# Optimization experiments

Measured on AMD Instinct MI355X. Metric: run time of the kernel, lower is better.

The kernel has to match this reference:

```python
import jax, jax.numpy as jnp
import numpy as np

B, N, D = 4, 4096, 1024
H, HD = 16, 64            # num_heads, head_dim (dim // num_heads)
K_ANCHOR = 256
SCALE = 1.0 / np.sqrt(float(HD))


def setup_inputs() -> dict:
    key = jax.random.key(0)
    ks = jax.random.split(key, 12)
    init = lambda k, shape, fan_in: jax.random.normal(k, shape, jnp.float32) * (1.0 / np.sqrt(fan_in))
    return {
        "x": jax.random.normal(ks[0], (B, N, D), jnp.float32),
        "Wq": init(ks[1], (D, H * HD), D), "bq": jnp.zeros((H * HD,), jnp.float32),
        "Wk": init(ks[2], (D, H * HD), D), "bk": jnp.zeros((H * HD,), jnp.float32),
        "Wv": init(ks[3], (D, H * HD), D), "bv": jnp.zeros((H * HD,), jnp.float32),
        "Wqt": init(ks[4], (D, D), D),     "bqt": jnp.zeros((D,), jnp.float32),
        "Wo": init(ks[5], (H * HD, D), H * HD), "bo": jnp.zeros((D,), jnp.float32),
        "num_anchor_tokens": K_ANCHOR,
    }


def _split_heads(t):
    # [B, S, H*HD] -> [B, H, S, HD]
    b, s, _ = t.shape
    return t.reshape(b, s, H, HD).transpose(0, 2, 1, 3)


def reference(x, Wq, bq, Wk, bk, Wv, bv, Wqt, bqt, Wo, bo, num_anchor_tokens):
    K = num_anchor_tokens  # static python int
    anchors = x[:, :K]     # [B, K, D]
    queries = x[:, K:]     # [B, N-K, D]

    q_a = anchors @ Wq + bq           # [B, K, H*HD]
    k_a = anchors @ Wk + bk           # [B, K, H*HD]
    v_a = anchors @ Wv + bv           # [B, K, H*HD]
    q_q = queries @ Wqt + bqt         # [B, N-K, H*HD] (dim == H*HD)

    q = _split_heads(jnp.concatenate([q_a, q_q], axis=1))  # [B, H, N, HD]
    k = _split_heads(k_a)                                  # [B, H, K, HD]
    v = _split_heads(v_a)                                  # [B, H, K, HD]

    scores = jnp.einsum("bhnd,bhkd->bhnk", q, k) * SCALE   # [B, H, N, K]
    weights = jax.nn.softmax(scores, axis=-1)
    ctx = jnp.einsum("bhnk,bhkd->bhnd", weights, v)        # [B, H, N, HD]
    ctx = ctx.transpose(0, 2, 1, 3).reshape(x.shape[0], x.shape[1], H * HD)
    return ctx @ Wo + bo               # [B, N, D]
```

## Files before the change

kernel.cpp:

```cpp
#include <hip/hip_runtime.h>
#include <stdint.h>
#include <stddef.h>


typedef _Float16 v8hf __attribute__((ext_vector_type(8)));
typedef _Float16 h4   __attribute__((ext_vector_type(4)));
typedef float    f32x4 __attribute__((ext_vector_type(4)));
typedef uint32_t u32x4 __attribute__((ext_vector_type(4)));

#define ATT_SCALE 0.125f
#define LOG2E     1.44269504088896340736f
#define QK_CE     (ATT_SCALE * LOG2E)

__device__ __forceinline__ void async16(const void* g, void* l) {
  __builtin_amdgcn_global_load_lds(
      (const __attribute__((address_space(1))) void*)g,
      (__attribute__((address_space(3))) void*)l,
      16, 0, 0);
}

__device__ __forceinline__ uint32_t pk_h2(float a, float b) {
  auto w = __builtin_amdgcn_cvt_pkrtz(a, b);
  return __builtin_bit_cast(uint32_t, w);
}

__global__ __launch_bounds__(256) void cvt_kernel(const float* __restrict__ src,
                                                  _Float16* __restrict__ dst, int n) {
  int i = (blockIdx.x * 256 + threadIdx.x) * 4;
  if (i + 3 < n) {
    float4 v = *(const float4*)(src + i);
    h4 o; o[0] = (_Float16)v.x; o[1] = (_Float16)v.y; o[2] = (_Float16)v.z; o[3] = (_Float16)v.w;
    *(h4*)(dst + i) = o;
  }
}

struct TPArgs { const float* src[5]; _Float16* dst[5]; };

__global__ __launch_bounds__(256) void transpose5_k(TPArgs a) {
  __shared__ _Float16 t[32][33];
  const int z = blockIdx.z;
  const float* __restrict__ src = a.src[z];
  _Float16* __restrict__ dst = a.dst[z];
  const int bx = blockIdx.x * 32, by = blockIdx.y * 32;
  const int x = threadIdx.x;
  for (int yy = threadIdx.y; yy < 32; yy += 8)
    t[yy][x] = (_Float16)src[(size_t)(by + yy) * 1024 + bx + x];
  __syncthreads();
  for (int yy = threadIdx.y; yy < 32; yy += 8)
    dst[(size_t)(bx + yy) * 1024 + by + x] = t[x][yy];
}

template <typename OutT>
__global__ __launch_bounds__(512, 2) void gemm256(
    const _Float16* __restrict__ A, const _Float16* __restrict__ Bt,
    const float* __restrict__ bias, OutT* __restrict__ out,
    int rowsPerBatch, int rowStart, float oscale)
{
  __shared__ __attribute__((aligned(16))) _Float16 As[4 * 256 * 32];
  __shared__ __attribute__((aligned(16))) _Float16 Bs[4 * 256 * 32];

  const int tid  = threadIdx.x;
  const int wave = tid >> 6, lane = tid & 63;
  const int quad = lane >> 4, l16 = lane & 15;
  const int wr = wave >> 2, wc = wave & 3;

  const int nwg = gridDim.x * gridDim.y;
  const int lin = blockIdx.y * 4 + blockIdx.x;
  const int swz = (lin & 7) * (nwg >> 3) + (lin >> 3);
  const int bx = swz & 3, by = swz >> 2;

  const int lrow = lane >> 2, lblk = lane & 3;

  auto gRowOf = [&](int m) -> int {
    int b = m / rowsPerBatch;
    return b * 4096 + rowStart + (m - b * rowsPerBatch);
  };

  const int tr0 = wave * 16 + lrow;
  const int tr1 = 128 + tr0;
  const _Float16* aS0 = A  + (size_t)gRowOf(by * 256 + tr0) * 1024 + (lblk ^ ((tr0 >> 1) & 3)) * 8;
  const _Float16* aS1 = A  + (size_t)gRowOf(by * 256 + tr1) * 1024 + (lblk ^ ((tr1 >> 1) & 3)) * 8;
  const _Float16* bS0 = Bt + (size_t)(bx * 256 + tr0) * 1024 + (lblk ^ ((tr0 >> 1) & 3)) * 8;
  const _Float16* bS1 = Bt + (size_t)(bx * 256 + tr1) * 1024 + (lblk ^ ((tr1 >> 1) & 3)) * 8;

  auto stageA = [&](int t) {
    const int k0 = t * 32;
    _Float16* ad = As + (t & 3) * 8192 + wave * 512;
    async16(aS0 + k0, ad);
    async16(aS1 + k0, ad + 4096);
  };
  auto stageB = [&](int t) {
    const int k0 = t * 32;
    _Float16* bd = Bs + (t & 3) * 8192 + wave * 512;
    async16(bS0 + k0, bd);
    async16(bS1 + k0, bd + 4096);
  };

  const int fblk = (quad ^ ((l16 >> 1) & 3)) * 8;

  f32x4 acc[8][4];
  #pragma unroll
  for (int i = 0; i < 8; i++)
    #pragma unroll
    for (int j = 0; j < 4; j++)
      acc[i][j] = f32x4{0.f, 0.f, 0.f, 0.f};

  stageA(0); stageB(0); stageA(1); stageB(1); stageA(2); stageB(2);
  asm volatile("s_waitcnt vmcnt(8)" ::: "memory");
  __builtin_amdgcn_s_barrier();

  #pragma unroll 1
  for (int t = 0; t < 32; ++t) {
    const _Float16* Ab = As + (t & 3) * 8192;
    const _Float16* Bb = Bs + (t & 3) * 8192;
    v8hf af0[4], af1[4], bf[4];

    #pragma unroll
    for (int nt = 0; nt < 4; nt++)
      bf[nt] = *(const v8hf*)(Bb + (wc * 64 + nt * 16 + l16) * 32 + fblk);
    #pragma unroll
    for (int mt = 0; mt < 4; mt++)
      af0[mt] = *(const v8hf*)(Ab + (wr * 128 + mt * 16 + l16) * 32 + fblk);
    if (t + 3 < 32) stageA(t + 3);
    __builtin_amdgcn_s_barrier();
    asm volatile("s_waitcnt lgkmcnt(0)" ::: "memory");
    __builtin_amdgcn_sched_barrier(0);
    __builtin_amdgcn_s_setprio(1);
    #pragma unroll
    for (int mt = 0; mt < 4; mt++)
      #pragma unroll
      for (int nt = 0; nt < 4; nt++)
        acc[mt][nt] = __builtin_amdgcn_mfma_f32_16x16x32_f16(af0[mt], bf[nt], acc[mt][nt], 0, 0, 0);
    __builtin_amdgcn_s_setprio(0);
    __builtin_amdgcn_s_barrier();

    #pragma unroll
    for (int mt = 0; mt < 4; mt++)
      af1[mt] = *(const v8hf*)(Ab + (wr * 128 + (mt + 4) * 16 + l16) * 32 + fblk);
    if (t + 3 < 32) stageB(t + 3);
    if (t <= 28)      asm volatile("s_waitcnt vmcnt(6)" ::: "memory");
    else if (t == 29) asm volatile("s_waitcnt vmcnt(4)" ::: "memory");
    else              asm volatile("s_waitcnt vmcnt(0)" ::: "memory");
    __builtin_amdgcn_s_barrier();
    asm volatile("s_waitcnt lgkmcnt(0)" ::: "memory");
    __builtin_amdgcn_sched_barrier(0);
    __builtin_amdgcn_s_setprio(1);
    #pragma unroll
    for (int mt = 0; mt < 4; mt++)
      #pragma unroll
      for (int nt = 0; nt < 4; nt++)
        acc[mt + 4][nt] = __builtin_amdgcn_mfma_f32_16x16x32_f16(af1[mt], bf[nt], acc[mt + 4][nt], 0, 0, 0);
    __builtin_amdgcn_s_setprio(0);
    __builtin_amdgcn_s_barrier();
  }

  const int colBase = bx * 256 + wc * 64;
  const int rowBase = by * 256 + wr * 128;
  #pragma unroll
  for (int mt = 0; mt < 8; mt++) {
    #pragma unroll
    for (int r = 0; r < 4; r++) {
      int m = rowBase + mt * 16 + quad * 4 + r;
      int b = m / rowsPerBatch;
      int rr = m - b * rowsPerBatch;
      #pragma unroll
      for (int nt = 0; nt < 4; nt++) {
        int col = colBase + nt * 16 + l16;
        float v = (acc[mt][nt][r] + bias[col]) * oscale;
        out[(size_t)(b * 4096 + rowStart + rr) * 1024 + col] = (OutT)v;
      }
    }
  }
}

template <typename OutT>
__global__ __launch_bounds__(256) void gemm64(
    const _Float16* __restrict__ A, const _Float16* __restrict__ Bt,
    const float* __restrict__ bias0, const float* __restrict__ bias1,
    const float* __restrict__ bias2,
    OutT* __restrict__ out0, _Float16* __restrict__ out1, _Float16* __restrict__ out2,
    int rowsPerBatch, int rowStart, int mode)
{
  __shared__ __attribute__((aligned(16))) _Float16 As[64 * 32];
  __shared__ __attribute__((aligned(16))) _Float16 Bs[128 * 32];

  const int tid  = threadIdx.x;
  const int wave = tid >> 6, lane = tid & 63;
  const int quad = lane >> 4, l16 = lane & 15;
  const int wr = wave >> 1, wc = wave & 1;

  const int gx = gridDim.x;
  const int lin = blockIdx.y * gx + blockIdx.x;
  const int x8 = lin & 7, j = lin >> 3;
  const int bx = j % gx;
  const int by = x8 * (gridDim.y >> 3) + j / gx;

  const int srow = lane >> 2;
  const int skol = (((lane & 3) ^ ((lane >> 3) & 3)) * 8);

  auto gRowOf = [&](int m) -> int {
    int b = m / rowsPerBatch;
    int r = m - b * rowsPerBatch;
    return b * 4096 + rowStart + r;
  };

  const int bc0 = wave * 2, bc1 = bc0 + 1;
  const _Float16* aS  = A  + (size_t)gRowOf(by * 64 + wave * 16 + srow) * 1024 + skol;
  const _Float16* bS0 = Bt + (size_t)(bx * 128 + bc0 * 16 + srow) * 1024 + skol;
  const _Float16* bS1 = Bt + (size_t)(bx * 128 + bc1 * 16 + srow) * 1024 + skol;
  _Float16* aD  = As + wave * 512;
  _Float16* bD0 = Bs + bc0 * 512;
  _Float16* bD1 = Bs + bc1 * 512;

  const int fblk = (quad ^ ((l16 >> 1) & 3)) * 8;

  f32x4 acc[2][4];
  #pragma unroll
  for (int i = 0; i < 2; i++)
    #pragma unroll
    for (int jj = 0; jj < 4; jj++)
      acc[i][jj] = f32x4{0.f, 0.f, 0.f, 0.f};

  for (int k0 = 0; k0 < 1024; k0 += 32) {
    __syncthreads();
    async16(aS  + k0, aD);
    async16(bS0 + k0, bD0);
    async16(bS1 + k0, bD1);
    __syncthreads();

    v8hf af[2], bfr[4];
    #pragma unroll
    for (int mt = 0; mt < 2; mt++)
      af[mt] = *(const v8hf*)(As + (wr * 32 + mt * 16 + l16) * 32 + fblk);
    #pragma unroll
    for (int nt = 0; nt < 4; nt++)
      bfr[nt] = *(const v8hf*)(Bs + (wc * 64 + nt * 16 + l16) * 32 + fblk);
    #pragma unroll
    for (int mt = 0; mt < 2; mt++)
      #pragma unroll
      for (int nt = 0; nt < 4; nt++)
        acc[mt][nt] = __builtin_amdgcn_mfma_f32_16x16x32_f16(af[mt], bfr[nt], acc[mt][nt], 0, 0, 0);
  }

  const int colBase = bx * 128 + wc * 64;
  const int rowBase = by * 64 + wr * 32;
  #pragma unroll
  for (int mt = 0; mt < 2; mt++) {
    #pragma unroll
    for (int r = 0; r < 4; r++) {
      int m = rowBase + mt * 16 + quad * 4 + r;
      int b = m / rowsPerBatch;
      int rr = m - b * rowsPerBatch;
      #pragma unroll
      for (int nt = 0; nt < 4; nt++) {
        int col = colBase + nt * 16 + l16;
        float v = acc[mt][nt][r];
        if (mode == 0) {
          v += bias0[col];
          out0[(size_t)(b * 4096 + rowStart + rr) * 1024 + col] = (OutT)v;
        } else {
          if (col < 1024) {
            v = (v + bias0[col]) * QK_CE;
            out0[(size_t)(b * 4096 + rr) * 1024 + col] = (OutT)v;
          } else if (col < 2048) {
            int c2 = col - 1024;
            v += bias1[c2];
            out1[(size_t)(b * 256 + rr) * 1024 + c2] = (_Float16)v;
          } else {
            int c2 = col - 2048;
            v += bias2[c2];
            int hh = c2 >> 6, d = c2 & 63;
            int kk = ((rr >> 7) & 1) * 128 + (rr & 15) * 8 + ((rr >> 4) & 7);
            int idx = ((kk >> 5) * 4 + (d >> 4)) * 512
                    + (((kk >> 3) & 3) * 16 + (d & 15)) * 8 + (kk & 7);
            out2[(size_t)(b * 16 + hh) * 16384 + idx] = (_Float16)v;
          }
        }
      }
    }
  }
}

__global__ __launch_bounds__(256, 5) void attn_kernel(
    const _Float16* __restrict__ q, const _Float16* __restrict__ k,
    const _Float16* __restrict__ vt, _Float16* __restrict__ ctx)
{
  __shared__ __attribute__((aligned(16))) _Float16 KP[256 * 64];

  const int tid  = threadIdx.x;
  const int wave = tid >> 6, lane = tid & 63;
  const int quad = lane >> 4, l16 = lane & 15;
  const int bid = blockIdx.x;
  const int qt = bid & 63, h = (bid >> 6) & 15, b = bid >> 10;

  const int fq = (l16 ^ (l16 >> 1)) & 7;

  const _Float16* kbase = k + (size_t)b * 256 * 1024 + h * 64;
  {
    const int s = lane >> 3;
    const int p = lane & 7;
    #pragma unroll
    for (int i = 0; i < 8; i++) {
      int c = wave * 8 + i;
      int row = c * 8 + s;
      int f = (row ^ (row >> 1)) & 7;
      async16(kbase + (size_t)row * 1024 + (p ^ f) * 8, KP + c * 512);
    }
  }

  const int qrow = qt * 64 + wave * 16 + l16;
  const _Float16* qbase = q + (size_t)(b * 4096 + qrow) * 1024 + h * 64 + quad * 8;
  v8hf a0 = *(const v8hf*)(qbase);
  v8hf a1 = *(const v8hf*)(qbase + 32);

  f32x4 s[16];
  #pragma unroll
  for (int t = 0; t < 16; t++) s[t] = f32x4{0.f, 0.f, 0.f, 0.f};

  __syncthreads();

  #pragma unroll
  for (int t = 0; t < 16; t++) {
    const _Float16* rbase = KP + (t * 16 + l16) * 64;
    int pb0 = (quad ^ fq) * 8;
    v8hf b0 = *(const v8hf*)(rbase + pb0);
    v8hf b1 = *(const v8hf*)(rbase + (pb0 ^ 32));
    s[t] = __builtin_amdgcn_mfma_f32_16x16x32_f16(a0, b0, s[t], 0, 0, 0);
    s[t] = __builtin_amdgcn_mfma_f32_16x16x32_f16(a1, b1, s[t], 0, 0, 0);
  }

  float inv[4];
  #pragma unroll
  for (int r = 0; r < 4; r++) {
    float sum = 0.f;
    #pragma unroll
    for (int t = 0; t < 16; t++) {
      float e = __builtin_amdgcn_exp2f(s[t][r]);
      s[t][r] = e;
      sum += e;
    }
    sum += __shfl_xor(sum, 1);
    sum += __shfl_xor(sum, 2);
    sum += __shfl_xor(sum, 4);
    sum += __shfl_xor(sum, 8);
    inv[r] = 1.0f / sum;
  }

  __syncthreads();

  #pragma unroll
  for (int r = 0; r < 4; r++) {
    const int qr = quad * 4 + r;
    const int fp = (qr ^ (qr >> 1)) & 7;
    _Float16* prow = KP + (wave * 16 + qr) * 256;
    u32x4 lo, hi;
    #pragma unroll
    for (int j = 0; j < 4; j++) {
      lo[j] = pk_h2(s[2 * j][r],     s[2 * j + 1][r]);
      hi[j] = pk_h2(s[2 * j + 8][r], s[2 * j + 9][r]);
    }
    *(u32x4*)(prow + (l16 ^ fp) * 8)        = lo;
    *(u32x4*)(prow + ((l16 ^ fp) + 16) * 8) = hi;
  }

  asm volatile("s_waitcnt lgkmcnt(0)" ::: "memory");
  __builtin_amdgcn_sched_barrier(0);

  const _Float16* vlane = vt + (size_t)(b * 16 + h) * 16384 + lane * 8;
  f32x4 o[4];
  #pragma unroll
  for (int nt = 0; nt < 4; nt++) o[nt] = f32x4{0.f, 0.f, 0.f, 0.f};
  #pragma unroll
  for (int c = 0; c < 8; c++) {
    v8hf pa = *(const v8hf*)(KP + (wave * 16 + l16) * 256 + ((c * 4 + quad) ^ fq) * 8);
    #pragma unroll
    for (int nt = 0; nt < 4; nt++) {
      v8hf vb = *(const v8hf*)(vlane + (c * 4 + nt) * 512);
      o[nt] = __builtin_amdgcn_mfma_f32_16x16x32_f16(pa, vb, o[nt], 0, 0, 0);
    }
  }

  _Float16* obase = ctx + (size_t)(b * 4096 + qt * 64 + wave * 16 + quad * 4) * 1024 + h * 64;
  #pragma unroll
  for (int nt = 0; nt < 4; nt++)
    #pragma unroll
    for (int r = 0; r < 4; r++)
      obase[(size_t)r * 1024 + nt * 16 + l16] = (_Float16)(o[nt][r] * inv[r]);
}

extern "C" void kernel_launch(void* const* d_in, const int* in_sizes, int n_in,
                              void* d_out, int out_size, void* d_ws, size_t ws_size,
                              hipStream_t stream)
{
  (void)in_sizes; (void)n_in; (void)out_size; (void)ws_size;

  const float* x   = (const float*)d_in[0];
  const float* Wq  = (const float*)d_in[1];
  const float* bq  = (const float*)d_in[2];
  const float* Wk  = (const float*)d_in[3];
  const float* bk  = (const float*)d_in[4];
  const float* Wv  = (const float*)d_in[5];
  const float* bv  = (const float*)d_in[6];
  const float* Wqt = (const float*)d_in[7];
  const float* bqt = (const float*)d_in[8];
  const float* Wo  = (const float*)d_in[9];
  const float* bo  = (const float*)d_in[10];

  char* ws = (char*)d_ws;
  _Float16* xh    = (_Float16*)(ws);
  _Float16* WtQKV = (_Float16*)(ws + (32ll << 20));
  _Float16* WtQT  = (_Float16*)(ws + (38ll << 20));
  _Float16* WtO   = (_Float16*)(ws + (40ll << 20));
  _Float16* qbuf  = (_Float16*)(ws + (42ll << 20));
  _Float16* kbuf  = (_Float16*)(ws + (74ll << 20));
  _Float16* vtb   = (_Float16*)(ws + (76ll << 20));
  _Float16* ctxb  = (_Float16*)(ws + (78ll << 20));
  float* outp = (float*)d_out;

  const int nx = 4 * 4096 * 1024;
  cvt_kernel<<<nx / 1024, 256, 0, stream>>>(x, xh, nx);

  TPArgs tpa;
  tpa.src[0] = Wq;  tpa.dst[0] = WtQKV;
  tpa.src[1] = Wk;  tpa.dst[1] = WtQKV + 1024 * 1024;
  tpa.src[2] = Wv;  tpa.dst[2] = WtQKV + 2 * 1024 * 1024;
  tpa.src[3] = Wqt; tpa.dst[3] = WtQT;
  tpa.src[4] = Wo;  tpa.dst[4] = WtO;
  transpose5_k<<<dim3(32, 32, 5), dim3(32, 8), 0, stream>>>(tpa);

  gemm64<_Float16><<<dim3(24, 16), 256, 0, stream>>>(xh, WtQKV, bq, bk, bv,
                                                     qbuf, kbuf, vtb, 256, 0, 1);
  gemm256<_Float16><<<dim3(4, 60), 512, 0, stream>>>(xh, WtQT, bqt,
                                                     qbuf, 3840, 256, QK_CE);
  attn_kernel<<<4096, 256, 0, stream>>>(qbuf, kbuf, vtb, ctxb);
  gemm256<float><<<dim3(4, 64), 512, 0, stream>>>(ctxb, WtO, bo,
                                                  outp, 4096, 0, 1.0f);
}
```

Baseline: 289.2 us.

## Merge prep kernels and fuse anchor QKV and query projections into one GEMM launch

```diff
diff --git a/kernel.cpp b/kernel.cpp
--- a/kernel.cpp
+++ b/kernel.cpp
@@ -24,30 +24,32 @@
   return __builtin_bit_cast(uint32_t, w);
 }
 
-__global__ __launch_bounds__(256) void cvt_kernel(const float* __restrict__ src,
-                                                  _Float16* __restrict__ dst, int n) {
-  int i = (blockIdx.x * 256 + threadIdx.x) * 4;
-  if (i + 3 < n) {
-    float4 v = *(const float4*)(src + i);
+struct TPArgs { const float* src[5]; _Float16* dst[5]; };
+
+__global__ __launch_bounds__(256) void prep_kernel(
+    const float* __restrict__ x, _Float16* __restrict__ xh, TPArgs a)
+{
+  __shared__ _Float16 t[32][33];
+  const int bid = blockIdx.x;
+  if (bid < 16384) {
+    int i = (bid * 256 + threadIdx.x) * 4;
+    float4 v = *(const float4*)(x + i);
     h4 o; o[0] = (_Float16)v.x; o[1] = (_Float16)v.y; o[2] = (_Float16)v.z; o[3] = (_Float16)v.w;
-    *(h4*)(dst + i) = o;
-  }
-}
-
-struct TPArgs { const float* src[5]; _Float16* dst[5]; };
-
-__global__ __launch_bounds__(256) void transpose5_k(TPArgs a) {
-  __shared__ _Float16 t[32][33];
-  const int z = blockIdx.z;
-  const float* __restrict__ src = a.src[z];
-  _Float16* __restrict__ dst = a.dst[z];
-  const int bx = blockIdx.x * 32, by = blockIdx.y * 32;
-  const int x = threadIdx.x;
-  for (int yy = threadIdx.y; yy < 32; yy += 8)
-    t[yy][x] = (_Float16)src[(size_t)(by + yy) * 1024 + bx + x];
-  __syncthreads();
-  for (int yy = threadIdx.y; yy < 32; yy += 8)
-    dst[(size_t)(bx + yy) * 1024 + by + x] = t[x][yy];
+    *(h4*)(xh + i) = o;
+  } else {
+    const int tb = bid - 16384;
+    const int z = tb >> 10;
+    const int rem = tb & 1023;
+    const int bxx = (rem & 31) * 32, byy = (rem >> 5) * 32;
+    const float* __restrict__ src = a.src[z];
+    _Float16* __restrict__ dst = a.dst[z];
+    const int xx = threadIdx.x & 31, ty = threadIdx.x >> 5;
+    for (int yy = ty; yy < 32; yy += 8)
+      t[yy][xx] = (_Float16)src[(size_t)(byy + yy) * 1024 + bxx + xx];
+    __syncthreads();
+    for (int yy = ty; yy < 32; yy += 8)
+      dst[(size_t)(bxx + yy) * 1024 + byy + xx] = t[xx][yy];
+  }
 }
 
 template <typename OutT>
@@ -173,79 +175,123 @@
   }
 }
 
-template <typename OutT>
-__global__ __launch_bounds__(256) void gemm64(
-    const _Float16* __restrict__ A, const _Float16* __restrict__ Bt,
-    const float* __restrict__ bias0, const float* __restrict__ bias1,
-    const float* __restrict__ bias2,
-    OutT* __restrict__ out0, _Float16* __restrict__ out1, _Float16* __restrict__ out2,
-    int rowsPerBatch, int rowStart, int mode)
+__global__ __launch_bounds__(512, 2) void gemm_qkv(
+    const _Float16* __restrict__ xh,
+    const _Float16* __restrict__ WtQT, const _Float16* __restrict__ WtQKV,
+    const float* __restrict__ bqt, const float* __restrict__ bq,
+    const float* __restrict__ bk, const float* __restrict__ bv,
+    _Float16* __restrict__ qout, _Float16* __restrict__ kout,
+    _Float16* __restrict__ vout)
 {
-  __shared__ __attribute__((aligned(16))) _Float16 As[64 * 32];
-  __shared__ __attribute__((aligned(16))) _Float16 Bs[128 * 32];
+  __shared__ __attribute__((aligned(16))) _Float16 As[4 * 256 * 32];
+  __shared__ __attribute__((aligned(16))) _Float16 Bs[4 * 256 * 32];
 
   const int tid  = threadIdx.x;
   const int wave = tid >> 6, lane = tid & 63;
   const int quad = lane >> 4, l16 = lane & 15;
-  const int wr = wave >> 1, wc = wave & 1;
-
-  const int gx = gridDim.x;
-  const int lin = blockIdx.y * gx + blockIdx.x;
-  const int x8 = lin & 7, j = lin >> 3;
-  const int bx = j % gx;
-  const int by = x8 * (gridDim.y >> 3) + j / gx;
-
-  const int srow = lane >> 2;
-  const int skol = (((lane & 3) ^ ((lane >> 3) & 3)) * 8);
+  const int wr = wave >> 2, wc = wave & 3;
+
+  const int nwg = gridDim.x;
+  const int lin = blockIdx.x;
+  const int swz = (lin & 7) * (nwg >> 3) + (lin >> 3);
+  const bool anch = swz >= 240;
+  const int id = anch ? (swz - 240) : swz;
+  const int bx = anch ? (id % 12) : (id & 3);
+  const int by = anch ? (id / 12) : (id >> 2);
+
+  const _Float16* __restrict__ Bt = anch ? WtQKV : WtQT;
+  const int rowsPerBatch = anch ? 256 : 3840;
+  const int rowStart     = anch ? 0 : 256;
+
+  const int lrow = lane >> 2, lblk = lane & 3;
 
   auto gRowOf = [&](int m) -> int {
     int b = m / rowsPerBatch;
-    int r = m - b * rowsPerBatch;
-    return b * 4096 + rowStart + r;
-  };
-
-  const int bc0 = wave * 2, bc1 = bc0 + 1;
-  const _Float16* aS  = A  + (size_t)gRowOf(by * 64 + wave * 16 + srow) * 1024 + skol;
-  const _Float16* bS0 = Bt + (size_t)(bx * 128 + bc0 * 16 + srow) * 1024 + skol;
-  const _Float16* bS1 = Bt + (size_t)(bx * 128 + bc1 * 16 + srow) * 1024 + skol;
-  _Float16* aD  = As + wave * 512;
-  _Float16* bD0 = Bs + bc0 * 512;
-  _Float16* bD1 = Bs + bc1 * 512;
+    return b * 4096 + rowStart + (m - b * rowsPerBatch);
+  };
+
+  const int tr0 = wave * 16 + lrow;
+  const int tr1 = 128 + tr0;
+  const _Float16* aS0 = xh + (size_t)gRowOf(by * 256 + tr0) * 1024 + (lblk ^ ((tr0 >> 1) & 3)) * 8;
+  const _Float16* aS1 = xh + (size_t)gRowOf(by * 256 + tr1) * 1024 + (lblk ^ ((tr1 >> 1) & 3)) * 8;
+  const _Float16* bS0 = Bt + (size_t)(bx * 256 + tr0) * 1024 + (lblk ^ ((tr0 >> 1) & 3)) * 8;
+  const _Float16* bS1 = Bt + (size_t)(bx * 256 + tr1) * 1024 + (lblk ^ ((tr1 >> 1) & 3)) * 8;
+
+  auto stageA = [&](int t) {
+    const int k0 = t * 32;
+    _Float16* ad = As + (t & 3) * 8192 + wave * 512;
+    async16(aS0 + k0, ad);
+    async16(aS1 + k0, ad + 4096);
+  };
+  auto stageB = [&](int t) {
+    const int k0 = t * 32;
+    _Float16* bd = Bs + (t & 3) * 8192 + wave * 512;
+    async16(bS0 + k0, bd);
+    async16(bS1 + k0, bd + 4096);
+  };
 
   const int fblk = (quad ^ ((l16 >> 1) & 3)) * 8;
 
-  f32x4 acc[2][4];
-  #pragma unroll
-  for (int i = 0; i < 2; i++)
-    #pragma unroll
-    for (int jj = 0; jj < 4; jj++)
-      acc[i][jj] = f32x4{0.f, 0.f, 0.f, 0.f};
-
-  for (int k0 = 0; k0 < 1024; k0 += 32) {
-    __syncthreads();
-    async16(aS  + k0, aD);
-    async16(bS0 + k0, bD0);
-    async16(bS1 + k0, bD1);
-    __syncthreads();
-
-    v8hf af[2], bfr[4];
-    #pragma unroll
-    for (int mt = 0; mt < 2; mt++)
-      af[mt] = *(const v8hf*)(As + (wr * 32 + mt * 16 + l16) * 32 + fblk);
+  f32x4 acc[8][4];
+  #pragma unroll
+  for (int i = 0; i < 8; i++)
+    #pragma unroll
+    for (int j = 0; j < 4; j++)
+      acc[i][j] = f32x4{0.f, 0.f, 0.f, 0.f};
+
+  stageA(0); stageB(0); stageA(1); stageB(1); stageA(2); stageB(2);
+  asm volatile("s_waitcnt vmcnt(8)" ::: "memory");
+  __builtin_amdgcn_s_barrier();
+
+  #pragma unroll 1
+  for (int t = 0; t < 32; ++t) {
+    const _Float16* Ab = As + (t & 3) * 8192;
+    const _Float16* Bb = Bs + (t & 3) * 8192;
+    v8hf af0[4], af1[4], bf[4];
+
     #pragma unroll
     for (int nt = 0; nt < 4; nt++)
-      bfr[nt] = *(const v8hf*)(Bs + (wc * 64 + nt * 16 + l16) * 32 + fblk);
-    #pragma unroll
-    for (int mt = 0; mt < 2; mt++)
+      bf[nt] = *(const v8hf*)(Bb + (wc * 64 + nt * 16 + l16) * 32 + fblk);
+    #pragma unroll
+    for (int mt = 0; mt < 4; mt++)
+      af0[mt] = *(const v8hf*)(Ab + (wr * 128 + mt * 16 + l16) * 32 + fblk);
+    if (t + 3 < 32) stageA(t + 3);
+    __builtin_amdgcn_s_barrier();
+    asm volatile("s_waitcnt lgkmcnt(0)" ::: "memory");
+    __builtin_amdgcn_sched_barrier(0);
+    __builtin_amdgcn_s_setprio(1);
+    #pragma unroll
+    for (int mt = 0; mt < 4; mt++)
       #pragma unroll
       for (int nt = 0; nt < 4; nt++)
-        acc[mt][nt] = __builtin_amdgcn_mfma_f32_16x16x32_f16(af[mt], bfr[nt], acc[mt][nt], 0, 0, 0);
-  }
-
-  const int colBase = bx * 128 + wc * 64;
-  const int rowBase = by * 64 + wr * 32;
-  #pragma unroll
-  for (int mt = 0; mt < 2; mt++) {
+        acc[mt][nt] = __builtin_amdgcn_mfma_f32_16x16x32_f16(af0[mt], bf[nt], acc[mt][nt], 0, 0, 0);
+    __builtin_amdgcn_s_setprio(0);
+    __builtin_amdgcn_s_barrier();
+
+    #pragma unroll
+    for (int mt = 0; mt < 4; mt++)
+      af1[mt] = *(const v8hf*)(Ab + (wr * 128 + (mt + 4) * 16 + l16) * 32 + fblk);
+    if (t + 3 < 32) stageB(t + 3);
+    if (t <= 28)      asm volatile("s_waitcnt vmcnt(6)" ::: "memory");
+    else if (t == 29) asm volatile("s_waitcnt vmcnt(4)" ::: "memory");
+    else              asm volatile("s_waitcnt vmcnt(0)" ::: "memory");
+    __builtin_amdgcn_s_barrier();
+    asm volatile("s_waitcnt lgkmcnt(0)" ::: "memory");
+    __builtin_amdgcn_sched_barrier(0);
+    __builtin_amdgcn_s_setprio(1);
+    #pragma unroll
+    for (int mt = 0; mt < 4; mt++)
+      #pragma unroll
+      for (int nt = 0; nt < 4; nt++)
+        acc[mt + 4][nt] = __builtin_amdgcn_mfma_f32_16x16x32_f16(af1[mt], bf[nt], acc[mt + 4][nt], 0, 0, 0);
+    __builtin_amdgcn_s_setprio(0);
+    __builtin_amdgcn_s_barrier();
+  }
+
+  const int colBase = bx * 256 + wc * 64;
+  const int rowBase = by * 256 + wr * 128;
+  #pragma unroll
+  for (int mt = 0; mt < 8; mt++) {
     #pragma unroll
     for (int r = 0; r < 4; r++) {
       int m = rowBase + mt * 16 + quad * 4 + r;
@@ -255,25 +301,25 @@
       for (int nt = 0; nt < 4; nt++) {
         int col = colBase + nt * 16 + l16;
         float v = acc[mt][nt][r];
-        if (mode == 0) {
-          v += bias0[col];
-          out0[(size_t)(b * 4096 + rowStart + rr) * 1024 + col] = (OutT)v;
+        if (!anch) {
+          v = (v + bqt[col]) * QK_CE;
+          qout[(size_t)(b * 4096 + 256 + rr) * 1024 + col] = (_Float16)v;
         } else {
           if (col < 1024) {
-            v = (v + bias0[col]) * QK_CE;
-            out0[(size_t)(b * 4096 + rr) * 1024 + col] = (OutT)v;
+            v = (v + bq[col]) * QK_CE;
+            qout[(size_t)(b * 4096 + rr) * 1024 + col] = (_Float16)v;
           } else if (col < 2048) {
             int c2 = col - 1024;
-            v += bias1[c2];
-            out1[(size_t)(b * 256 + rr) * 1024 + c2] = (_Float16)v;
+            v += bk[c2];
+            kout[(size_t)(b * 256 + rr) * 1024 + c2] = (_Float16)v;
           } else {
             int c2 = col - 2048;
-            v += bias2[c2];
+            v += bv[c2];
             int hh = c2 >> 6, d = c2 & 63;
             int kk = ((rr >> 7) & 1) * 128 + (rr & 15) * 8 + ((rr >> 4) & 7);
             int idx = ((kk >> 5) * 4 + (d >> 4)) * 512
                     + (((kk >> 3) & 3) * 16 + (d & 15)) * 8 + (kk & 7);
-            out2[(size_t)(b * 16 + hh) * 16384 + idx] = (_Float16)v;
+            vout[(size_t)(b * 16 + hh) * 16384 + idx] = (_Float16)v;
           }
         }
       }
@@ -417,22 +463,20 @@
   _Float16* ctxb  = (_Float16*)(ws + (78ll << 20));
   float* outp = (float*)d_out;
 
-  const int nx = 4 * 4096 * 1024;
-  cvt_kernel<<<nx / 1024, 256, 0, stream>>>(x, xh, nx);
-
   TPArgs tpa;
   tpa.src[0] = Wq;  tpa.dst[0] = WtQKV;
   tpa.src[1] = Wk;  tpa.dst[1] = WtQKV + 1024 * 1024;
   tpa.src[2] = Wv;  tpa.dst[2] = WtQKV + 2 * 1024 * 1024;
   tpa.src[3] = Wqt; tpa.dst[3] = WtQT;
   tpa.src[4] = Wo;  tpa.dst[4] = WtO;
-  transpose5_k<<<dim3(32, 32, 5), dim3(32, 8), 0, stream>>>(tpa);
-
-  gemm64<_Float16><<<dim3(24, 16), 256, 0, stream>>>(xh, WtQKV, bq, bk, bv,
-                                                     qbuf, kbuf, vtb, 256, 0, 1);
-  gemm256<_Float16><<<dim3(4, 60), 512, 0, stream>>>(xh, WtQT, bqt,
-                                                     qbuf, 3840, 256, QK_CE);
+
+  prep_kernel<<<16384 + 5120, 256, 0, stream>>>(x, xh, tpa);
+
+  gemm_qkv<<<288, 512, 0, stream>>>(xh, WtQT, WtQKV, bqt, bq, bk, bv,
+                                    qbuf, kbuf, vtb);
+
   attn_kernel<<<4096, 256, 0, stream>>>(qbuf, kbuf, vtb, ctxb);
+
   gemm256<float><<<dim3(4, 64), 512, 0, stream>>>(ctxb, WtO, bo,
                                                   outp, 4096, 0, 1.0f);
 }
```

Result: slower. 339.1 us (+17.2%).
